# Performance work log

Hardware: AMD Instinct MI355X
Metric: run time of the kernel (lower is better)

## Reference

```python
import jax, jax.numpy as jnp
import numpy as np

EPS_CB = 1e-6   # ConvBlock BN eps (partial(nn.BatchNorm2d, eps=1e-6))
EPS_BN = 1e-5   # default nn.BatchNorm2d / BatchNorm1d eps


def conv2d(x, w, stride=1, pad=0):
    return jax.lax.conv_general_dilated(
        x, w, (stride, stride), [(pad, pad), (pad, pad)],
        dimension_numbers=('NCHW', 'OIHW', 'NCHW'))


def bn2d(x, g, b, m, v, eps):
    inv = (g / jnp.sqrt(v + eps)).reshape(1, -1, 1, 1)
    return (x - m.reshape(1, -1, 1, 1)) * inv + b.reshape(1, -1, 1, 1)


def setup_inputs() -> dict:
    key = jax.random.key(0)
    ks = iter(jax.random.split(key, 40))
    B, C, H, W = 16, 512, 64, 64
    K = 64                 # num_codes (hard-coded to 64 in __init__)
    c4 = C // 4            # bottleneck width in ConvBlock (expansion=4)

    def w_(shape, scale=0.05):
        return jax.random.normal(next(ks), shape, jnp.float32) * scale

    def bnp(n):
        return (jax.random.uniform(next(ks), (n,), jnp.float32, 0.5, 1.5),  # gamma
                w_((n,), 0.05),                                            # beta
                w_((n,), 0.05),                                            # running mean
                jax.random.uniform(next(ks), (n,), jnp.float32, 0.5, 1.5)) # running var

    g1, b1, m1, v1 = bnp(c4)
    g2, b2, m2, v2 = bnp(c4)
    g3, b3, m3, v3 = bnp(C)
    gr, br, mr, vr = bnp(C)
    gl, bl, ml, vl = bnp(C)
    ge, be, me, ve = bnp(K)

    std = 1.0 / np.sqrt(K * C)
    inp = {
        'x': jax.random.normal(next(ks), (B, C, H, W), jnp.float32),
        # ConvBlock
        'w1': w_((c4, C, 1, 1)), 'g1': g1, 'b1': b1, 'm1': m1, 'v1': v1,
        'w2': w_((c4, c4, 3, 3)), 'g2': g2, 'b2': b2, 'm2': m2, 'v2': v2,
        'w3': w_((C, c4, 1, 1)), 'g3': g3, 'b3': b3, 'm3': m3, 'v3': v3,
        'wr': w_((C, C, 1, 1)), 'gr': gr, 'br': br, 'mr': mr, 'vr': vr,
        # LVC 1x1 conv + BN2d
        'wl': w_((C, C, 1, 1)), 'gl': gl, 'bl': bl, 'ml': ml, 'vl': vl,
        # Encoding
        'codewords': jax.random.uniform(next(ks), (K, C), jnp.float32, -std, std),
        'scale': jax.random.uniform(next(ks), (K,), jnp.float32, -1.0, 0.0),
        # BN1d over codes
        'ge': ge, 'be': be, 'me': me, 've': ve,
        # fc gate
        'wfc': w_((C, C)), 'bfc': w_((C,), 0.05),
    }
    return inp


def lvc_forward(x, w1, g1, b1, m1, v1, w2, g2, b2, m2, v2, w3, g3, b3, m3, v3,
                wr, gr, br, mr, vr, wl, gl, bl, ml, vl, codewords, scale,
                ge, be, me, ve, wfc, bfc):
    # ---- ConvBlock (bottleneck with 1x1 residual), eval-mode BN ----
    h = jax.nn.relu(bn2d(conv2d(x, w1), g1, b1, m1, v1, EPS_CB))
    h = jax.nn.relu(bn2d(conv2d(h, w2, pad=1), g2, b2, m2, v2, EPS_CB))
    h = jax.nn.relu(bn2d(conv2d(h, w3), g3, b3, m3, v3, EPS_CB))
    res = bn2d(conv2d(x, wr), gr, br, mr, vr, EPS_CB)
    x1 = h + res                                   # (B, C, H, W)

    # ---- LVC: 1x1 conv + BN + ReLU ----
    y = jax.nn.relu(bn2d(conv2d(x1, wl), gl, bl, ml, vl, EPS_BN))

    # ---- Encoding: scaled L2 -> softmax over codes -> aggregate ----
    B, C, H, W = y.shape
    xf = y.reshape(B, C, H * W).transpose(0, 2, 1)     # (B, N, C)
    x_sq = jnp.sum(xf * xf, axis=-1, keepdims=True)    # (B, N, 1)
    c_sq = jnp.sum(codewords * codewords, axis=-1)     # (K,)
    xc = jnp.einsum('bnc,kc->bnk', xf, codewords)      # (B, N, K)
    dist = scale * (x_sq - 2.0 * xc + c_sq)            # (B, N, K)
    A = jax.nn.softmax(dist, axis=2)                   # assignment weights
    # sum_n A[b,n,k] * (x[b,n,:] - codewords[k,:])  -> (B, K, C)
    enc = jnp.einsum('bnk,bnc->bkc', A, xf) - A.sum(axis=1)[..., None] * codewords

    # ---- BN1d over num_codes dim + ReLU + mean over codes ----
    inv = (ge / jnp.sqrt(ve + EPS_BN)).reshape(1, -1, 1)
    enc = (enc - me.reshape(1, -1, 1)) * inv + be.reshape(1, -1, 1)
    en = jax.nn.relu(enc).mean(axis=1)                 # (B, C)

    # ---- SE-style gate ----
    gam = jax.nn.sigmoid(en @ wfc.T + bfc)             # (B, C)
    gate = gam.reshape(B, C, 1, 1)
    return jax.nn.relu(x1 + x1 * gate)


def reference(x, w1, g1, b1, m1, v1, w2, g2, b2, m2, v2, w3, g3, b3, m3, v3,
              wr, gr, br, mr, vr, wl, gl, bl, ml, vl, codewords, scale,
              ge, be, me, ve, wfc, bfc):
    return lvc_forward(x, w1, g1, b1, m1, v1, w2, g2, b2, m2, v2,
                       w3, g3, b3, m3, v3, wr, gr, br, mr, vr,
                       wl, gl, bl, ml, vl, codewords, scale,
                       ge, be, me, ve, wfc, bfc)
```

## Files before the change

### kernel.cpp

```cpp
#include <hip/hip_runtime.h>
#include <math.h>

typedef float f32x4 __attribute__((ext_vector_type(4)));
typedef short s16x8 __attribute__((ext_vector_type(8)));
typedef unsigned short u16x4 __attribute__((ext_vector_type(4)));

#define HW 4096
#define CCH 512
#define NK 64
#define EPAD 136

#define C_XB   0ULL
#define C_H2   67108864ULL
#define C_H1P  83886080ULL
#define C_X1B  83886080ULL
#define C_YB   0ULL
#define C_AHI  67108864ULL
#define C_ALO  75497472ULL
#define C_ASUM 150994944ULL
#define C_GAM  150999040ULL
#define C_MISC 151031808ULL
#define C_W1F  151048192ULL
#define C_W2F  151179264ULL
#define C_W3B  151474176ULL
#define C_WRB  151605248ULL
#define C_WLB  152129536ULL
#define C_PE   152653824ULL

#define MS_S1 0
#define MS_T1 128
#define MS_S2 256
#define MS_T2 384
#define MS_S3 512
#define MS_T3 1024
#define MS_SR 1536
#define MS_TR 2048
#define MS_SL 2560
#define MS_TL 3072
#define MS_SE 3584
#define MS_TE 3648
#define MS_CSQ 3712

__device__ __forceinline__ float b2f(unsigned short u) {
  unsigned int x = ((unsigned int)u) << 16;
  return __builtin_bit_cast(float, x);
}
__device__ __forceinline__ unsigned short f2b(float f) {
  unsigned int i = __builtin_bit_cast(unsigned int, f);
  i += 0x7fffu + ((i >> 16) & 1u);
  return (unsigned short)(i >> 16);
}

__global__ void prep_kernel(
    const float* __restrict__ g1, const float* __restrict__ b1, const float* __restrict__ m1, const float* __restrict__ v1,
    const float* __restrict__ g2, const float* __restrict__ b2, const float* __restrict__ m2, const float* __restrict__ v2,
    const float* __restrict__ g3, const float* __restrict__ b3, const float* __restrict__ m3, const float* __restrict__ v3,
    const float* __restrict__ gr, const float* __restrict__ br, const float* __restrict__ mr, const float* __restrict__ vr,
    const float* __restrict__ gl, const float* __restrict__ bl, const float* __restrict__ ml, const float* __restrict__ vl,
    const float* __restrict__ ge, const float* __restrict__ be, const float* __restrict__ me, const float* __restrict__ ve,
    const float* __restrict__ cw, float* __restrict__ misc)
{
  const int t = threadIdx.x;
  if (t < 128) {
    float s = g1[t] * rsqrtf(v1[t] + 1e-6f);
    misc[MS_S1 + t] = s; misc[MS_T1 + t] = b1[t] - m1[t] * s;
    s = g2[t] * rsqrtf(v2[t] + 1e-6f);
    misc[MS_S2 + t] = s; misc[MS_T2 + t] = b2[t] - m2[t] * s;
  }
  for (int c = t; c < 512; c += 256) {
    float s = g3[c] * rsqrtf(v3[c] + 1e-6f);
    misc[MS_S3 + c] = s; misc[MS_T3 + c] = b3[c] - m3[c] * s;
    s = gr[c] * rsqrtf(vr[c] + 1e-6f);
    misc[MS_SR + c] = s; misc[MS_TR + c] = br[c] - mr[c] * s;
    s = gl[c] * rsqrtf(vl[c] + 1e-5f);
    misc[MS_SL + c] = s; misc[MS_TL + c] = bl[c] - ml[c] * s;
  }
  if (t < 64) {
    float s = ge[t] * rsqrtf(ve[t] + 1e-5f);
    misc[MS_SE + t] = s; misc[MS_TE + t] = be[t] - me[t] * s;
    float acc = 0.f;
    for (int c = 0; c < 512; ++c) { float v = cw[t * 512 + c]; acc += v * v; }
    misc[MS_CSQ + t] = acc;
  }
}

__global__ void fold_bf16_kernel(const float* __restrict__ w, const float* __restrict__ s,
                                 unsigned short* __restrict__ out, int total, int kper)
{
  int i = blockIdx.x * 256 + threadIdx.x;
  if (i < total) out[i] = f2b(w[i] * s[i / kper]);
}

__global__ void fold_w2_kernel(const float* __restrict__ w2, const float* __restrict__ s,
                               unsigned short* __restrict__ out)
{
  int j = blockIdx.x * 256 + threadIdx.x;
  if (j < 147456) {
    int m = j / 1152, r = j - m * 1152;
    int tp = r >> 7, ci = r & 127;
    out[j] = f2b(w2[m * 1152 + ci * 9 + tp] * s[m]);
  }
}

__global__ __launch_bounds__(256) void tr_kernel(const float* __restrict__ x,
                                                 unsigned short* __restrict__ xb)
{
  __shared__ float T[64][65];
  const int b = blockIdx.z, c0 = blockIdx.y * 64, n0 = blockIdx.x * 64;
  const int t = threadIdx.x;
  const int rr = t >> 4, cc = (t & 15) * 4;
#pragma unroll
  for (int rep = 0; rep < 4; ++rep) {
    const int cr = rep * 16 + rr;
    const float4 v = *(const float4*)(x + ((size_t)(b * 512 + c0 + cr)) * 4096 + n0 + cc);
    T[cr][cc + 0] = v.x; T[cr][cc + 1] = v.y; T[cr][cc + 2] = v.z; T[cr][cc + 3] = v.w;
  }
  __syncthreads();
#pragma unroll
  for (int rep = 0; rep < 4; ++rep) {
    const int nr = rep * 16 + rr;
    u16x4 o;
    o[0] = f2b(T[cc + 0][nr]); o[1] = f2b(T[cc + 1][nr]);
    o[2] = f2b(T[cc + 2][nr]); o[3] = f2b(T[cc + 3][nr]);
    *(u16x4*)(xb + ((size_t)(b * 4096 + n0 + nr)) * 512 + c0 + cc) = o;
  }
}


template<int BMODE>
__device__ __forceinline__ void run_phase(
    const unsigned short* __restrict__ Wp,
    const unsigned short* __restrict__ Xb,
    const int K, const int tid, const int n0,
    unsigned short* __restrict__ As, unsigned short* __restrict__ Bs,
    f32x4 acc[4][4])
{
  const int lane = tid & 63;
  const int wv = tid >> 6, wm = wv >> 1, wn = wv & 1;

  const int ko = tid & 3;
  const int r0 = tid >> 2;
  const int r1 = 64 + r0;

  const unsigned short* aS0 = Wp + (size_t)r0 * K + ko * 8;
  const unsigned short* aS1 = Wp + (size_t)r1 * K + ko * 8;
  const int slot0 = (((r0 >> 4) * 64) + ko * 16 + (r0 & 15)) * 8;
  const int slot1 = (((r1 >> 4) * 64) + ko * 16 + (r1 & 15)) * 8;

  const unsigned short* bS0 = nullptr;
  const unsigned short* bS1 = nullptr;
  size_t bBase0 = 0, bBase1 = 0;
  if constexpr (BMODE == 0) {
    bS0 = Xb + (size_t)(n0 + r0) * K + ko * 8;
    bS1 = Xb + (size_t)(n0 + r1) * K + ko * 8;
  } else {
    const int pg0 = n0 + r0, pg1 = n0 + r1;
    bBase0 = (size_t)((pg0 >> 6) * 66 + (pg0 & 63)) * 128 + ko * 8;
    bBase1 = (size_t)((pg1 >> 6) * 66 + (pg1 & 63)) * 128 + ko * 8;
  }

  s16x8 a0, a1, b0, b1;
  auto LOADC = [&](int kt) {
    __builtin_memcpy(&a0, aS0 + kt, 16);
    __builtin_memcpy(&a1, aS1 + kt, 16);
    if constexpr (BMODE == 0) {
      __builtin_memcpy(&b0, bS0 + kt, 16);
      __builtin_memcpy(&b1, bS1 + kt, 16);
    } else {
      const int tap = kt >> 7;
      const int ky = tap / 3, kx = tap - ky * 3;
      const int off = (ky * 66 + kx) * 128 + (kt & 127);
      __builtin_memcpy(&b0, Xb + bBase0 + off, 16);
      __builtin_memcpy(&b1, Xb + bBase1 + off, 16);
    }
  };

  LOADC(0);
  *(s16x8*)(As + slot0) = a0; *(s16x8*)(As + slot1) = a1;
  *(s16x8*)(Bs + slot0) = b0; *(s16x8*)(Bs + slot1) = b1;
  __syncthreads();

  int cur = 0;
  for (int kt = 0; kt < K; kt += 32) {
    const bool more = (kt + 32) < K;
    if (more) LOADC(kt + 32);

    const unsigned short* Ac = As + cur * 4096;
    const unsigned short* Bc = Bs + cur * 4096;
    s16x8 afr[4], bfr[4];
#pragma unroll
    for (int i = 0; i < 4; ++i)
      afr[i] = *(const s16x8*)(Ac + (size_t)((wm * 4 + i) * 64 + lane) * 8);
#pragma unroll
    for (int j = 0; j < 4; ++j)
      bfr[j] = *(const s16x8*)(Bc + (size_t)((wn * 4 + j) * 64 + lane) * 8);
#pragma unroll
    for (int i = 0; i < 4; ++i)
#pragma unroll
      for (int j = 0; j < 4; ++j)
        acc[i][j] = __builtin_amdgcn_mfma_f32_16x16x32_bf16(afr[i], bfr[j], acc[i][j], 0, 0, 0);

    if (more) {
      const int nx = (cur ^ 1) * 4096;
      *(s16x8*)(As + nx + slot0) = a0; *(s16x8*)(As + nx + slot1) = a1;
      *(s16x8*)(Bs + nx + slot0) = b0; *(s16x8*)(Bs + nx + slot1) = b1;
    }
    __syncthreads();
    cur ^= 1;
  }
}

template<int BMODE, bool DUAL>
__global__ __launch_bounds__(256) void mgemm_kernel(
    const unsigned short* __restrict__ W0, const unsigned short* __restrict__ X0,
    const int K0, const long long xbs0,
    const unsigned short* __restrict__ W1, const unsigned short* __restrict__ X1,
    const int Kp1, const long long xbs1,
    const float* __restrict__ biasMid, const float* __restrict__ biasOut,
    const int omode, const int reluF, const int ldm,
    unsigned short* __restrict__ outB, const long long obsB)
{
  __shared__ __align__(16) unsigned short smem[128 * EPAD];
  unsigned short* As = smem;
  unsigned short* Bs = smem + 8192;

  const int tid = threadIdx.x;
  const int b = blockIdx.z;
  const int n0 = blockIdx.x * 128;
  const int m0 = blockIdx.y * 128;
  const int lane = tid & 63, wv = tid >> 6, wm = wv >> 1, wn = wv & 1;
  const int q = lane >> 4, mm = lane & 15;

  f32x4 acc[4][4];
#pragma unroll
  for (int i = 0; i < 4; ++i)
#pragma unroll
    for (int j = 0; j < 4; ++j) acc[i][j] = (f32x4){0.f, 0.f, 0.f, 0.f};

  run_phase<BMODE>(W0 + (size_t)m0 * K0, X0 + (size_t)b * xbs0, K0, tid, n0, As, Bs, acc);

  if constexpr (DUAL) {
#pragma unroll
    for (int i = 0; i < 4; ++i) {
      const int mb = m0 + wm * 64 + i * 16 + q * 4;
#pragma unroll
      for (int r = 0; r < 4; ++r) {
        const float bm = biasMid[mb + r];
#pragma unroll
        for (int j = 0; j < 4; ++j) acc[i][j][r] = fmaxf(acc[i][j][r] + bm, 0.f);
      }
    }
    run_phase<0>(W1 + (size_t)m0 * Kp1, X1 + (size_t)b * xbs1, Kp1, tid, n0, As, Bs, acc);
  }

  __syncthreads();
  if (omode == 3) {
#pragma unroll
    for (int i = 0; i < 4; ++i) {
      const int chb = wm * 64 + i * 16 + q * 4;
#pragma unroll
      for (int r = 0; r < 4; ++r) {
        const float bo = biasOut[m0 + chb + r];
#pragma unroll
        for (int j = 0; j < 4; ++j) {
          const int px = wn * 64 + j * 16 + mm;
          float v = acc[i][j][r] + bo;
          if (reluF) v = fmaxf(v, 0.f);
          smem[(size_t)(chb + r) * EPAD + px] = f2b(v);
        }
      }
    }
    __syncthreads();
    const int ch = tid >> 1, half = tid & 1;
    const unsigned short* src = smem + (size_t)ch * EPAD + half * 64;
    unsigned short* dst = outB + (size_t)b * obsB + (size_t)(m0 + ch) * HW + n0 + half * 64;
#pragma unroll
    for (int r = 0; r < 8; ++r) {
      s16x8 v;
      __builtin_memcpy(&v, src + r * 8, 16);
      *(s16x8*)(dst + r * 8) = v;
    }
  } else {
#pragma unroll
    for (int i = 0; i < 4; ++i) {
      const int chb = wm * 64 + i * 16 + q * 4;
      float bo[4];
#pragma unroll
      for (int r = 0; r < 4; ++r) bo[r] = biasOut[m0 + chb + r];
#pragma unroll
      for (int j = 0; j < 4; ++j) {
        const int px = wn * 64 + j * 16 + mm;
        u16x4 o;
#pragma unroll
        for (int r = 0; r < 4; ++r) {
          float v = acc[i][j][r] + bo[r];
          if (reluF) v = fmaxf(v, 0.f);
          o[r] = f2b(v);
        }
        *(u16x4*)(smem + (size_t)px * EPAD + chb) = o;
      }
    }
    __syncthreads();
    const int px = tid >> 1, half = tid & 1;
    const unsigned short* src = smem + (size_t)px * EPAD + half * 64;
    size_t dstoff;
    if (omode == 1) {
      dstoff = (size_t)b * obsB + (size_t)(n0 + px) * ldm + m0 + half * 64;
    } else {
      const int hp = ((n0 + px) >> 6) + 1, wp = ((n0 + px) & 63) + 1;
      dstoff = (size_t)b * obsB + ((size_t)hp * 66 + wp) * 128 + m0 + half * 64;
    }
    unsigned short* dst = outB + dstoff;
#pragma unroll
    for (int r = 0; r < 8; ++r) {
      s16x8 v;
      __builtin_memcpy(&v, src + r * 8, 16);
      *(s16x8*)(dst + r * 8) = v;
    }
  }
}

__global__ __launch_bounds__(256) void assign_kernel(
    const unsigned short* __restrict__ Yv, const float* __restrict__ cw, const float* __restrict__ scale,
    const float* __restrict__ misc, unsigned short* __restrict__ Ahi, unsigned short* __restrict__ Alo)
{
  __shared__ float Cs[16][64];
  __shared__ float Ys[16][64];
  __shared__ float dist[64][65];
  __shared__ float red[4][64];
  __shared__ float xsq[64];
  __shared__ float scl[64];
  __shared__ float csq[64];
  const int tid = threadIdx.x;
  const int b  = blockIdx.y;
  const int n0 = blockIdx.x * 64;
  if (tid < 64) { scl[tid] = scale[tid]; csq[tid] = misc[MS_CSQ + tid]; }
  const unsigned short* __restrict__ Yb = Yv + (size_t)b * CCH * HW;
  const int tr = tid >> 4, tc = tid & 15;
  const int lc_k = tid >> 2, lc_c = (tid & 3) * 4;
  const int ly_c0 = tid >> 6, ly_n = tid & 63;

  float acc[4][4];
#pragma unroll
  for (int i = 0; i < 4; ++i)
#pragma unroll
    for (int j = 0; j < 4; ++j) acc[i][j] = 0.f;
  float sq = 0.f;

  for (int c0 = 0; c0 < 512; c0 += 16) {
    const float4 cv = *(const float4*)(cw + (size_t)lc_k * 512 + c0 + lc_c);
    float yv[4];
#pragma unroll
    for (int rr = 0; rr < 4; ++rr)
      yv[rr] = b2f(Yb[(size_t)(c0 + ly_c0 + rr * 4) * HW + n0 + ly_n]);
    __syncthreads();
    Cs[lc_c + 0][lc_k] = cv.x;
    Cs[lc_c + 1][lc_k] = cv.y;
    Cs[lc_c + 2][lc_k] = cv.z;
    Cs[lc_c + 3][lc_k] = cv.w;
#pragma unroll
    for (int rr = 0; rr < 4; ++rr) {
      Ys[ly_c0 + rr * 4][ly_n] = yv[rr];
      sq += yv[rr] * yv[rr];
    }
    __syncthreads();
#pragma unroll
    for (int ct = 0; ct < 16; ++ct) {
      float rk[4], rn[4];
#pragma unroll
      for (int i = 0; i < 4; ++i) rk[i] = Cs[ct][tr * 4 + i];
#pragma unroll
      for (int j = 0; j < 4; ++j) rn[j] = Ys[ct][tc * 4 + j];
#pragma unroll
      for (int i = 0; i < 4; ++i)
#pragma unroll
        for (int j = 0; j < 4; ++j) acc[i][j] += rk[i] * rn[j];
    }
  }
  __syncthreads();
  red[ly_c0][ly_n] = sq;
  __syncthreads();
  if (tid < 64) xsq[tid] = red[0][tid] + red[1][tid] + red[2][tid] + red[3][tid];
  __syncthreads();
#pragma unroll
  for (int i = 0; i < 4; ++i)
#pragma unroll
    for (int j = 0; j < 4; ++j) {
      const int k = tr * 4 + i, n = tc * 4 + j;
      dist[k][n] = scl[k] * (xsq[n] - 2.f * acc[i][j] + csq[k]);
    }
  __syncthreads();
  const int qq = tid >> 6, n = tid & 63;
  float mx = -3.0e38f;
#pragma unroll
  for (int kk = 0; kk < 16; ++kk) mx = fmaxf(mx, dist[qq * 16 + kk][n]);
  red[qq][n] = mx;
  __syncthreads();
  mx = fmaxf(fmaxf(red[0][n], red[1][n]), fmaxf(red[2][n], red[3][n]));
  __syncthreads();
  float sum = 0.f;
#pragma unroll
  for (int kk = 0; kk < 16; ++kk) {
    const float e = __expf(dist[qq * 16 + kk][n] - mx);
    dist[qq * 16 + kk][n] = e;
    sum += e;
  }
  red[qq][n] = sum;
  __syncthreads();
  sum = red[0][n] + red[1][n] + red[2][n] + red[3][n];
  const float inv = 1.f / sum;
  const size_t base = (size_t)b * NK * HW + n0 + n;
#pragma unroll
  for (int kk = 0; kk < 16; ++kk) {
    const float a = dist[qq * 16 + kk][n] * inv;
    const unsigned short hi = f2b(a);
    const float rem = a - b2f(hi);
    Ahi[base + (size_t)(qq * 16 + kk) * HW] = hi;
    Alo[base + (size_t)(qq * 16 + kk) * HW] = f2b(rem);
  }
}

__global__ void asum_kernel(const unsigned short* __restrict__ Ahi,
                            const unsigned short* __restrict__ Alo, float* __restrict__ asum)
{
  const int bk = blockIdx.x;
  const unsigned short* __restrict__ rh = Ahi + (size_t)bk * HW;
  const unsigned short* __restrict__ rl = Alo + (size_t)bk * HW;
  const int t = threadIdx.x;
  float p = 0.f;
  for (int i = t * 8; i < HW; i += 2048) {
    s16x8 h, l;
    __builtin_memcpy(&h, rh + i, 16);
    __builtin_memcpy(&l, rl + i, 16);
#pragma unroll
    for (int e = 0; e < 8; ++e)
      p += b2f((unsigned short)h[e]) + b2f((unsigned short)l[e]);
  }
  __shared__ float sm[256];
  sm[t] = p;
  __syncthreads();
  for (int s = 128; s > 0; s >>= 1) {
    if (t < s) sm[t] += sm[t + s];
    __syncthreads();
  }
  if (t == 0) asum[bk] = sm[0];
}

__global__ __launch_bounds__(256) void enc_mfma_kernel(
    const unsigned short* __restrict__ Ahi, const unsigned short* __restrict__ Alo,
    const unsigned short* __restrict__ Yv, float* __restrict__ pe)
{
  __shared__ __align__(16) unsigned short AHs[2048];
  __shared__ __align__(16) unsigned short ALs[2048];
  __shared__ __align__(16) unsigned short Bs[4096];
  const int tid = threadIdx.x;
  const int ncol = blockIdx.x, nc = blockIdx.y, b = blockIdx.z;
  const int lane = tid & 63, wv = tid >> 6;
  const int q = lane >> 4, mm = lane & 15;

  const int ko = tid & 3;
  const int r  = tid >> 2;
  const size_t aoff = ((size_t)b * NK + r) * HW + nc * 1024 + ko * 8;
  const unsigned short* ahS = Ahi + aoff;
  const unsigned short* alS = Alo + aoff;
  const int slotA = (((r >> 4) * 64) + ko * 16 + (r & 15)) * 8;
  const unsigned short* b0S = Yv + ((size_t)b * CCH + ncol * 128 + r) * HW + nc * 1024 + ko * 8;
  const unsigned short* b1S = b0S + (size_t)64 * HW;
  const int slotB0 = (((r >> 4) * 64) + ko * 16 + (r & 15)) * 8;
  const int slotB1 = ((((r + 64) >> 4) * 64) + ko * 16 + (r & 15)) * 8;

  f32x4 acc[4][2];
#pragma unroll
  for (int i = 0; i < 4; ++i)
#pragma unroll
    for (int j = 0; j < 2; ++j) acc[i][j] = (f32x4){0.f, 0.f, 0.f, 0.f};

  for (int kt = 0; kt < 1024; kt += 32) {
    s16x8 ah, al, y0, y1;
    __builtin_memcpy(&ah, ahS + kt, 16);
    __builtin_memcpy(&al, alS + kt, 16);
    __builtin_memcpy(&y0, b0S + kt, 16);
    __builtin_memcpy(&y1, b1S + kt, 16);
    __syncthreads();
    *(s16x8*)(AHs + slotA) = ah;
    *(s16x8*)(ALs + slotA) = al;
    *(s16x8*)(Bs + slotB0) = y0;
    *(s16x8*)(Bs + slotB1) = y1;
    __syncthreads();

    s16x8 afh[4], afl[4], bfr[2];
#pragma unroll
    for (int i = 0; i < 4; ++i) {
      afh[i] = *(const s16x8*)(AHs + (size_t)(i * 64 + lane) * 8);
      afl[i] = *(const s16x8*)(ALs + (size_t)(i * 64 + lane) * 8);
    }
#pragma unroll
    for (int j = 0; j < 2; ++j)
      bfr[j] = *(const s16x8*)(Bs + (size_t)((wv * 2 + j) * 64 + lane) * 8);
#pragma unroll
    for (int i = 0; i < 4; ++i)
#pragma unroll
      for (int j = 0; j < 2; ++j) {
        acc[i][j] = __builtin_amdgcn_mfma_f32_16x16x32_bf16(afh[i], bfr[j], acc[i][j], 0, 0, 0);
        acc[i][j] = __builtin_amdgcn_mfma_f32_16x16x32_bf16(afl[i], bfr[j], acc[i][j], 0, 0, 0);
      }
  }

  float* __restrict__ peb = pe + ((size_t)(b * 4 + nc) * NK) * CCH;
#pragma unroll
  for (int i = 0; i < 4; ++i)
#pragma unroll
    for (int j = 0; j < 2; ++j) {
      const int c = ncol * 128 + (wv * 2 + j) * 16 + mm;
#pragma unroll
      for (int rr = 0; rr < 4; ++rr) {
        const int k = i * 16 + q * 4 + rr;
        peb[(size_t)k * CCH + c] = acc[i][j][rr];
      }
    }
}

__global__ __launch_bounds__(256) void engate_kernel(
    const float* __restrict__ pe, const float* __restrict__ asum, const float* __restrict__ cw,
    const float* __restrict__ misc, const float* __restrict__ wfc, const float* __restrict__ bfc,
    float* __restrict__ gam)
{
  const int b = blockIdx.x;
  const int t = threadIdx.x;
  __shared__ float asum_s[64], se_s[64], te_s[64];
  __shared__ __align__(16) float en_s[512];
  if (t < 64) {
    asum_s[t] = asum[b * 64 + t];
    se_s[t]   = misc[MS_SE + t];
    te_s[t]   = misc[MS_TE + t];
  }
  __syncthreads();
  for (int rep = 0; rep < 2; ++rep) {
    const int c = t + rep * 256;
    float en = 0.f;
    const float* __restrict__ peb = pe + (size_t)b * 4 * NK * CCH + c;
    for (int k = 0; k < 64; ++k) {
      const float ps = peb[(size_t)k * CCH] + peb[(size_t)(64 + k) * CCH] +
                       peb[(size_t)(128 + k) * CCH] + peb[(size_t)(192 + k) * CCH];
      float v = ps - asum_s[k] * cw[k * 512 + c];
      v = v * se_s[k] + te_s[k];
      en += fmaxf(v, 0.f);
    }
    en_s[c] = en * (1.f / 64.f);
  }
  __syncthreads();
  for (int rep = 0; rep < 2; ++rep) {
    const int i = t + rep * 256;
    float a = bfc[i];
    const float4* __restrict__ wrow = (const float4*)(wfc + (size_t)i * 512);
    const float4* __restrict__ ev = (const float4*)en_s;
    for (int j = 0; j < 128; ++j) {
      const float4 w4 = wrow[j];
      const float4 e4 = ev[j];
      a += w4.x * e4.x + w4.y * e4.y + w4.z * e4.z + w4.w * e4.w;
    }
    gam[b * 512 + i] = 1.f / (1.f + __expf(-a));
  }
}

__global__ __launch_bounds__(256) void fingate_kernel(
    const unsigned short* __restrict__ x1b, const float* __restrict__ gam,
    float* __restrict__ out)
{
  __shared__ float T[64][65];
  const int b = blockIdx.z, c0 = blockIdx.y * 64, n0 = blockIdx.x * 64;
  const int t = threadIdx.x;
  const int rr = t >> 4, cc = (t & 15) * 4;
#pragma unroll
  for (int rep = 0; rep < 4; ++rep) {
    const int pr = rep * 16 + rr;
    u16x4 v = *(const u16x4*)(x1b + ((size_t)(b * 4096 + n0 + pr)) * 512 + c0 + cc);
    T[cc + 0][pr] = b2f(v[0]);
    T[cc + 1][pr] = b2f(v[1]);
    T[cc + 2][pr] = b2f(v[2]);
    T[cc + 3][pr] = b2f(v[3]);
  }
  __syncthreads();
#pragma unroll
  for (int rep = 0; rep < 4; ++rep) {
    const int cr = rep * 16 + rr;
    const float g = 1.f + gam[b * 512 + c0 + cr];
    float4 o;
    o.x = fmaxf(T[cr][cc + 0] * g, 0.f);
    o.y = fmaxf(T[cr][cc + 1] * g, 0.f);
    o.z = fmaxf(T[cr][cc + 2] * g, 0.f);
    o.w = fmaxf(T[cr][cc + 3] * g, 0.f);
    *(float4*)(out + ((size_t)(b * 512 + c0 + cr)) * 4096 + n0 + cc) = o;
  }
}

extern "C" void kernel_launch(void* const* d_in, const int* in_sizes, int n_in,
                              void* d_out, int out_size, void* d_ws, size_t ws_size,
                              hipStream_t stream)
{
  const float* x  = (const float*)d_in[0];
  const float* w1 = (const float*)d_in[1];
  const float* g1 = (const float*)d_in[2];
  const float* b1 = (const float*)d_in[3];
  const float* m1 = (const float*)d_in[4];
  const float* v1 = (const float*)d_in[5];
  const float* w2 = (const float*)d_in[6];
  const float* g2 = (const float*)d_in[7];
  const float* b2 = (const float*)d_in[8];
  const float* m2 = (const float*)d_in[9];
  const float* v2 = (const float*)d_in[10];
  const float* w3 = (const float*)d_in[11];
  const float* g3 = (const float*)d_in[12];
  const float* b3 = (const float*)d_in[13];
  const float* m3 = (const float*)d_in[14];
  const float* v3 = (const float*)d_in[15];
  const float* wr = (const float*)d_in[16];
  const float* gr = (const float*)d_in[17];
  const float* br = (const float*)d_in[18];
  const float* mr = (const float*)d_in[19];
  const float* vr = (const float*)d_in[20];
  const float* wl = (const float*)d_in[21];
  const float* gl = (const float*)d_in[22];
  const float* bl = (const float*)d_in[23];
  const float* ml = (const float*)d_in[24];
  const float* vl = (const float*)d_in[25];
  const float* cw = (const float*)d_in[26];
  const float* scale = (const float*)d_in[27];
  const float* ge = (const float*)d_in[28];
  const float* be = (const float*)d_in[29];
  const float* me = (const float*)d_in[30];
  const float* ve = (const float*)d_in[31];
  const float* wfc = (const float*)d_in[32];
  const float* bfc = (const float*)d_in[33];

  char* wsb = (char*)d_ws;
  unsigned short* xb  = (unsigned short*)(wsb + C_XB);
  unsigned short* h2  = (unsigned short*)(wsb + C_H2);
  unsigned short* h1p = (unsigned short*)(wsb + C_H1P);
  unsigned short* x1b = (unsigned short*)(wsb + C_X1B);
  unsigned short* yb  = (unsigned short*)(wsb + C_YB);
  unsigned short* Ahi = (unsigned short*)(wsb + C_AHI);
  unsigned short* Alo = (unsigned short*)(wsb + C_ALO);
  float* pe   = (float*)(wsb + C_PE);
  float* asum = (float*)(wsb + C_ASUM);
  float* gam  = (float*)(wsb + C_GAM);
  float* misc = (float*)(wsb + C_MISC);
  unsigned short* w1f = (unsigned short*)(wsb + C_W1F);
  unsigned short* w2f = (unsigned short*)(wsb + C_W2F);
  unsigned short* w3b = (unsigned short*)(wsb + C_W3B);
  unsigned short* wrb = (unsigned short*)(wsb + C_WRB);
  unsigned short* wlb = (unsigned short*)(wsb + C_WLB);

  prep_kernel<<<1, 256, 0, stream>>>(g1, b1, m1, v1, g2, b2, m2, v2, g3, b3, m3, v3,
                                     gr, br, mr, vr, gl, bl, ml, vl, ge, be, me, ve,
                                     cw, misc);
  fold_bf16_kernel<<<256, 256, 0, stream>>>(w1, misc + MS_S1, w1f, 65536, 512);
  fold_w2_kernel<<<576, 256, 0, stream>>>(w2, misc + MS_S2, w2f);
  fold_bf16_kernel<<<256, 256, 0, stream>>>(w3, misc + MS_S3, w3b, 65536, 128);
  fold_bf16_kernel<<<1024, 256, 0, stream>>>(wr, misc + MS_SR, wrb, 262144, 512);
  fold_bf16_kernel<<<1024, 256, 0, stream>>>(wl, misc + MS_SL, wlb, 262144, 512);

  tr_kernel<<<dim3(64, 8, 16), 256, 0, stream>>>(x, xb);
  hipMemsetAsync(h1p, 0, 17842176, stream);

  mgemm_kernel<0, false><<<dim3(32, 1, 16), 256, 0, stream>>>(
      w1f, xb, 512, 4096LL * 512, nullptr, nullptr, 0, 0,
      nullptr, misc + MS_T1, 0, 1, 128, h1p, 4356LL * 128);
  mgemm_kernel<1, false><<<dim3(32, 1, 16), 256, 0, stream>>>(
      w2f, h1p, 1152, 4356LL * 128, nullptr, nullptr, 0, 0,
      nullptr, misc + MS_T2, 1, 1, 128, h2, 4096LL * 128);
  mgemm_kernel<0, true><<<dim3(32, 4, 16), 256, 0, stream>>>(
      w3b, h2, 128, 4096LL * 128, wrb, xb, 512, 4096LL * 512,
      misc + MS_T3, misc + MS_TR, 1, 0, 512, x1b, 4096LL * 512);
  mgemm_kernel<0, false><<<dim3(32, 4, 16), 256, 0, stream>>>(
      wlb, x1b, 512, 4096LL * 512, nullptr, nullptr, 0, 0,
      nullptr, misc + MS_TL, 3, 1, 0, yb, 512LL * 4096);

  assign_kernel<<<dim3(64, 16), 256, 0, stream>>>(yb, cw, scale, misc, Ahi, Alo);
  asum_kernel<<<1024, 256, 0, stream>>>(Ahi, Alo, asum);
  enc_mfma_kernel<<<dim3(4, 4, 16), 256, 0, stream>>>(Ahi, Alo, yb, pe);
  engate_kernel<<<16, 256, 0, stream>>>(pe, asum, cw, misc, wfc, bfc, gam);
  fingate_kernel<<<dim3(64, 8, 16), 256, 0, stream>>>(x1b, gam, (float*)d_out);
}
```

Baseline: 461.2 us.

## Widen GEMM block tile to 128x256 pixels with two-phase epilogue

Each GEMM block now covers 256 pixels instead of 128, so every warp accumulates a 4x8 grid of MFMA tiles and each A fragment is reused across twice as many B fragments. The B tile staging buffers grow to match, and the epilogue is split into two 128-pixel phases that reuse the existing shared-memory staging area. The goal is fewer global and LDS loads per MFMA. In exchange the accumulator footprint doubles, which raises register pressure and can lower occupancy, and the small M=128 GEMMs now launch only 256 blocks, which may underfill the GPU.

```diff
diff --git a/kernel.cpp b/kernel.cpp
--- a/kernel.cpp
+++ b/kernel.cpp
@@ -127,87 +127,104 @@
 }
 
 
+__device__ __forceinline__ void mfma_step(const unsigned short* __restrict__ Ac,
+                                          const unsigned short* __restrict__ Bc,
+                                          int lane, int wm, int wn, f32x4 acc[4][8])
+{
+  s16x8 afr[4], bfr[8];
+#pragma unroll
+  for (int i = 0; i < 4; ++i)
+    afr[i] = *(const s16x8*)(Ac + (size_t)((wm * 4 + i) * 64 + lane) * 8);
+#pragma unroll
+  for (int j = 0; j < 8; ++j)
+    bfr[j] = *(const s16x8*)(Bc + (size_t)((wn * 8 + j) * 64 + lane) * 8);
+#pragma unroll
+  for (int i = 0; i < 4; ++i)
+#pragma unroll
+    for (int j = 0; j < 8; ++j)
+      acc[i][j] = __builtin_amdgcn_mfma_f32_16x16x32_bf16(afr[i], bfr[j], acc[i][j], 0, 0, 0);
+}
+
 template<int BMODE>
 __device__ __forceinline__ void run_phase(
     const unsigned short* __restrict__ Wp,
     const unsigned short* __restrict__ Xb,
     const int K, const int tid, const int n0,
     unsigned short* __restrict__ As, unsigned short* __restrict__ Bs,
-    f32x4 acc[4][4])
+    f32x4 acc[4][8])
 {
   const int lane = tid & 63;
   const int wv = tid >> 6, wm = wv >> 1, wn = wv & 1;
 
   const int ko = tid & 3;
-  const int r0 = tid >> 2;
-  const int r1 = 64 + r0;
-
-  const unsigned short* aS0 = Wp + (size_t)r0 * K + ko * 8;
-  const unsigned short* aS1 = Wp + (size_t)r1 * K + ko * 8;
-  const int slot0 = (((r0 >> 4) * 64) + ko * 16 + (r0 & 15)) * 8;
-  const int slot1 = (((r1 >> 4) * 64) + ko * 16 + (r1 & 15)) * 8;
-
-  const unsigned short* bS0 = nullptr;
-  const unsigned short* bS1 = nullptr;
-  size_t bBase0 = 0, bBase1 = 0;
-  if constexpr (BMODE == 0) {
-    bS0 = Xb + (size_t)(n0 + r0) * K + ko * 8;
-    bS1 = Xb + (size_t)(n0 + r1) * K + ko * 8;
-  } else {
-    const int pg0 = n0 + r0, pg1 = n0 + r1;
-    bBase0 = (size_t)((pg0 >> 6) * 66 + (pg0 & 63)) * 128 + ko * 8;
-    bBase1 = (size_t)((pg1 >> 6) * 66 + (pg1 & 63)) * 128 + ko * 8;
-  }
-
-  s16x8 a0, a1, b0, b1;
-  auto LOADC = [&](int kt) {
-    __builtin_memcpy(&a0, aS0 + kt, 16);
-    __builtin_memcpy(&a1, aS1 + kt, 16);
+  const int rt = tid >> 2;
+  const unsigned short* aS0 = Wp + (size_t)rt * K + ko * 8;
+  const unsigned short* aS1 = Wp + (size_t)(64 + rt) * K + ko * 8;
+  const int slA0 = (((rt >> 4) * 64) + ko * 16 + (rt & 15)) * 8;
+  const int slA1 = ((((64 + rt) >> 4) * 64) + ko * 16 + (rt & 15)) * 8;
+
+  const unsigned short* bS[4];
+  size_t bBase[4];
+  int slB[4];
+#pragma unroll
+  for (int u = 0; u < 4; ++u) {
+    const int r = rt + u * 64;
+    slB[u] = (((r >> 4) * 64) + ko * 16 + (r & 15)) * 8;
     if constexpr (BMODE == 0) {
-      __builtin_memcpy(&b0, bS0 + kt, 16);
-      __builtin_memcpy(&b1, bS1 + kt, 16);
+      bS[u] = Xb + (size_t)(n0 + r) * K + ko * 8;
+      bBase[u] = 0;
     } else {
-      const int tap = kt >> 7;
-      const int ky = tap / 3, kx = tap - ky * 3;
-      const int off = (ky * 66 + kx) * 128 + (kt & 127);
-      __builtin_memcpy(&b0, Xb + bBase0 + off, 16);
-      __builtin_memcpy(&b1, Xb + bBase1 + off, 16);
-    }
-  };
+      const int pg = n0 + r;
+      bS[u] = nullptr;
+      bBase[u] = (size_t)((pg >> 6) * 66 + (pg & 63)) * 128 + ko * 8;
+    }
+  }
+
+  s16x8 a0, a1, bb0, bb1, bb2, bb3;
+#define LOADC(kt)                                                 \
+  {                                                               \
+    __builtin_memcpy(&a0, aS0 + (kt), 16);                        \
+    __builtin_memcpy(&a1, aS1 + (kt), 16);                        \
+    if constexpr (BMODE == 0) {                                   \
+      __builtin_memcpy(&bb0, bS[0] + (kt), 16);                   \
+      __builtin_memcpy(&bb1, bS[1] + (kt), 16);                   \
+      __builtin_memcpy(&bb2, bS[2] + (kt), 16);                   \
+      __builtin_memcpy(&bb3, bS[3] + (kt), 16);                   \
+    } else {                                                      \
+      const int tap_ = (kt) >> 7;                                 \
+      const int ky_ = tap_ / 3, kx_ = tap_ - ky_ * 3;             \
+      const int off_ = (ky_ * 66 + kx_) * 128 + ((kt) & 127);     \
+      __builtin_memcpy(&bb0, Xb + bBase[0] + off_, 16);           \
+      __builtin_memcpy(&bb1, Xb + bBase[1] + off_, 16);           \
+      __builtin_memcpy(&bb2, Xb + bBase[2] + off_, 16);           \
+      __builtin_memcpy(&bb3, Xb + bBase[3] + off_, 16);           \
+    }                                                             \
+  }
+#define WRITEC(Abuf, Bbuf)                                        \
+  {                                                               \
+    *(s16x8*)((Abuf) + slA0) = a0;                                \
+    *(s16x8*)((Abuf) + slA1) = a1;                                \
+    *(s16x8*)((Bbuf) + slB[0]) = bb0;                             \
+    *(s16x8*)((Bbuf) + slB[1]) = bb1;                             \
+    *(s16x8*)((Bbuf) + slB[2]) = bb2;                             \
+    *(s16x8*)((Bbuf) + slB[3]) = bb3;                             \
+  }
 
   LOADC(0);
-  *(s16x8*)(As + slot0) = a0; *(s16x8*)(As + slot1) = a1;
-  *(s16x8*)(Bs + slot0) = b0; *(s16x8*)(Bs + slot1) = b1;
+  WRITEC(As, Bs);
   __syncthreads();
 
   int cur = 0;
   for (int kt = 0; kt < K; kt += 32) {
     const bool more = (kt + 32) < K;
     if (more) LOADC(kt + 32);
-
-    const unsigned short* Ac = As + cur * 4096;
-    const unsigned short* Bc = Bs + cur * 4096;
-    s16x8 afr[4], bfr[4];
-#pragma unroll
-    for (int i = 0; i < 4; ++i)
-      afr[i] = *(const s16x8*)(Ac + (size_t)((wm * 4 + i) * 64 + lane) * 8);
-#pragma unroll
-    for (int j = 0; j < 4; ++j)
-      bfr[j] = *(const s16x8*)(Bc + (size_t)((wn * 4 + j) * 64 + lane) * 8);
-#pragma unroll
-    for (int i = 0; i < 4; ++i)
-#pragma unroll
-      for (int j = 0; j < 4; ++j)
-        acc[i][j] = __builtin_amdgcn_mfma_f32_16x16x32_bf16(afr[i], bfr[j], acc[i][j], 0, 0, 0);
-
-    if (more) {
-      const int nx = (cur ^ 1) * 4096;
-      *(s16x8*)(As + nx + slot0) = a0; *(s16x8*)(As + nx + slot1) = a1;
-      *(s16x8*)(Bs + nx + slot0) = b0; *(s16x8*)(Bs + nx + slot1) = b1;
-    }
+    mfma_step(As + cur * 4096, Bs + cur * 8192, lane, wm, wn, acc);
+    if (more) WRITEC(As + (cur ^ 1) * 4096, Bs + (cur ^ 1) * 8192);
     __syncthreads();
     cur ^= 1;
   }
+#undef LOADC
+#undef WRITEC
 }
 
 template<int BMODE, bool DUAL>
@@ -220,22 +237,22 @@
     const int omode, const int reluF, const int ldm,
     unsigned short* __restrict__ outB, const long long obsB)
 {
-  __shared__ __align__(16) unsigned short smem[128 * EPAD];
+  __shared__ __align__(16) unsigned short smem[24576];
   unsigned short* As = smem;
   unsigned short* Bs = smem + 8192;
 
   const int tid = threadIdx.x;
   const int b = blockIdx.z;
-  const int n0 = blockIdx.x * 128;
+  const int n0 = blockIdx.x * 256;
   const int m0 = blockIdx.y * 128;
   const int lane = tid & 63, wv = tid >> 6, wm = wv >> 1, wn = wv & 1;
   const int q = lane >> 4, mm = lane & 15;
 
-  f32x4 acc[4][4];
+  f32x4 acc[4][8];
 #pragma unroll
   for (int i = 0; i < 4; ++i)
 #pragma unroll
-    for (int j = 0; j < 4; ++j) acc[i][j] = (f32x4){0.f, 0.f, 0.f, 0.f};
+    for (int j = 0; j < 8; ++j) acc[i][j] = (f32x4){0.f, 0.f, 0.f, 0.f};
 
   run_phase<BMODE>(W0 + (size_t)m0 * K0, X0 + (size_t)b * xbs0, K0, tid, n0, As, Bs, acc);
 
@@ -247,75 +264,84 @@
       for (int r = 0; r < 4; ++r) {
         const float bm = biasMid[mb + r];
 #pragma unroll
-        for (int j = 0; j < 4; ++j) acc[i][j][r] = fmaxf(acc[i][j][r] + bm, 0.f);
+        for (int j = 0; j < 8; ++j) acc[i][j][r] = fmaxf(acc[i][j][r] + bm, 0.f);
       }
     }
     run_phase<0>(W1 + (size_t)m0 * Kp1, X1 + (size_t)b * xbs1, Kp1, tid, n0, As, Bs, acc);
   }
 
   __syncthreads();
-  if (omode == 3) {
-#pragma unroll
-    for (int i = 0; i < 4; ++i) {
-      const int chb = wm * 64 + i * 16 + q * 4;
-#pragma unroll
-      for (int r = 0; r < 4; ++r) {
-        const float bo = biasOut[m0 + chb + r];
-#pragma unroll
-        for (int j = 0; j < 4; ++j) {
-          const int px = wn * 64 + j * 16 + mm;
-          float v = acc[i][j][r] + bo;
-          if (reluF) v = fmaxf(v, 0.f);
-          smem[(size_t)(chb + r) * EPAD + px] = f2b(v);
+  for (int ph = 0; ph < 2; ++ph) {
+    if (omode == 3) {
+      if (wn == ph) {
+#pragma unroll
+        for (int i = 0; i < 4; ++i) {
+          const int chb = wm * 64 + i * 16 + q * 4;
+#pragma unroll
+          for (int r = 0; r < 4; ++r) {
+            const float bo = biasOut[m0 + chb + r];
+#pragma unroll
+            for (int j = 0; j < 8; ++j) {
+              const int px = j * 16 + mm;
+              float v = acc[i][j][r] + bo;
+              if (reluF) v = fmaxf(v, 0.f);
+              smem[(size_t)(chb + r) * EPAD + px] = f2b(v);
+            }
+          }
         }
       }
-    }
-    __syncthreads();
-    const int ch = tid >> 1, half = tid & 1;
-    const unsigned short* src = smem + (size_t)ch * EPAD + half * 64;
-    unsigned short* dst = outB + (size_t)b * obsB + (size_t)(m0 + ch) * HW + n0 + half * 64;
-#pragma unroll
-    for (int r = 0; r < 8; ++r) {
-      s16x8 v;
-      __builtin_memcpy(&v, src + r * 8, 16);
-      *(s16x8*)(dst + r * 8) = v;
-    }
-  } else {
-#pragma unroll
-    for (int i = 0; i < 4; ++i) {
-      const int chb = wm * 64 + i * 16 + q * 4;
-      float bo[4];
-#pragma unroll
-      for (int r = 0; r < 4; ++r) bo[r] = biasOut[m0 + chb + r];
-#pragma unroll
-      for (int j = 0; j < 4; ++j) {
-        const int px = wn * 64 + j * 16 + mm;
-        u16x4 o;
-#pragma unroll
-        for (int r = 0; r < 4; ++r) {
-          float v = acc[i][j][r] + bo[r];
-          if (reluF) v = fmaxf(v, 0.f);
-          o[r] = f2b(v);
+      __syncthreads();
+      const int ch = tid >> 1, half = tid & 1;
+      const unsigned short* src = smem + (size_t)ch * EPAD + half * 64;
+      unsigned short* dst = outB + (size_t)b * obsB + (size_t)(m0 + ch) * HW + n0 + ph * 128 + half * 64;
+#pragma unroll
+      for (int r = 0; r < 8; ++r) {
+        s16x8 v;
+        __builtin_memcpy(&v, src + r * 8, 16);
+        *(s16x8*)(dst + r * 8) = v;
+      }
+      __syncthreads();
+    } else {
+      if (wn == ph) {
+#pragma unroll
+        for (int i = 0; i < 4; ++i) {
+          const int chb = wm * 64 + i * 16 + q * 4;
+          float bo[4];
+#pragma unroll
+          for (int r = 0; r < 4; ++r) bo[r] = biasOut[m0 + chb + r];
+#pragma unroll
+          for (int j = 0; j < 8; ++j) {
+            const int px = j * 16 + mm;
+            u16x4 o;
+#pragma unroll
+            for (int r = 0; r < 4; ++r) {
+              float v = acc[i][j][r] + bo[r];
+              if (reluF) v = fmaxf(v, 0.f);
+              o[r] = f2b(v);
+            }
+            *(u16x4*)(smem + (size_t)px * EPAD + chb) = o;
+          }
         }
-        *(u16x4*)(smem + (size_t)px * EPAD + chb) = o;
       }
-    }
-    __syncthreads();
-    const int px = tid >> 1, half = tid & 1;
-    const unsigned short* src = smem + (size_t)px * EPAD + half * 64;
-    size_t dstoff;
-    if (omode == 1) {
-      dstoff = (size_t)b * obsB + (size_t)(n0 + px) * ldm + m0 + half * 64;
-    } else {
-      const int hp = ((n0 + px) >> 6) + 1, wp = ((n0 + px) & 63) + 1;
-      dstoff = (size_t)b * obsB + ((size_t)hp * 66 + wp) * 128 + m0 + half * 64;
-    }
-    unsigned short* dst = outB + dstoff;
-#pragma unroll
-    for (int r = 0; r < 8; ++r) {
-      s16x8 v;
-      __builtin_memcpy(&v, src + r * 8, 16);
-      *(s16x8*)(dst + r * 8) = v;
+      __syncthreads();
+      const int px = tid >> 1, half = tid & 1;
+      const int gpx = n0 + ph * 128 + px;
+      const unsigned short* src = smem + (size_t)px * EPAD + half * 64;
+      size_t dstoff;
+      if (omode == 1) {
+        dstoff = (size_t)b * obsB + (size_t)gpx * ldm + m0 + half * 64;
+      } else {
+        const int hp = (gpx >> 6) + 1, wp = (gpx & 63) + 1;
+        dstoff = (size_t)b * obsB + ((size_t)hp * 66 + wp) * 128 + m0 + half * 64;
+      }
+      unsigned short* dst = outB + dstoff;
+#pragma unroll
+      for (int r = 0; r < 8; ++r) {
+        s16x8 v;
+        __builtin_memcpy(&v, src + r * 8, 16);
+        *(s16x8*)(dst + r * 8) = v;
+      }
+      __syncthreads();
     }
   }
 }
@@ -663,16 +689,16 @@
   tr_kernel<<<dim3(64, 8, 16), 256, 0, stream>>>(x, xb);
   hipMemsetAsync(h1p, 0, 17842176, stream);
 
-  mgemm_kernel<0, false><<<dim3(32, 1, 16), 256, 0, stream>>>(
+  mgemm_kernel<0, false><<<dim3(16, 1, 16), 256, 0, stream>>>(
       w1f, xb, 512, 4096LL * 512, nullptr, nullptr, 0, 0,
       nullptr, misc + MS_T1, 0, 1, 128, h1p, 4356LL * 128);
-  mgemm_kernel<1, false><<<dim3(32, 1, 16), 256, 0, stream>>>(
+  mgemm_kernel<1, false><<<dim3(16, 1, 16), 256, 0, stream>>>(
       w2f, h1p, 1152, 4356LL * 128, nullptr, nullptr, 0, 0,
       nullptr, misc + MS_T2, 1, 1, 128, h2, 4096LL * 128);
-  mgemm_kernel<0, true><<<dim3(32, 4, 16), 256, 0, stream>>>(
+  mgemm_kernel<0, true><<<dim3(16, 4, 16), 256, 0, stream>>>(
       w3b, h2, 128, 4096LL * 128, wrb, xb, 512, 4096LL * 512,
       misc + MS_T3, misc + MS_TR, 1, 0, 512, x1b, 4096LL * 512);
-  mgemm_kernel<0, false><<<dim3(32, 4, 16), 256, 0, stream>>>(
+  mgemm_kernel<0, false><<<dim3(16, 4, 16), 256, 0, stream>>>(
       wlb, x1b, 512, 4096LL * 512, nullptr, nullptr, 0, 0,
       nullptr, misc + MS_TL, 3, 1, 0, yb, 512LL * 4096);
 
```

Measured after the change: 514.4 us. 11.5% more time.

## Compute code-assignment distances with bf16 MFMA using hi/lo split codewords

Applied to the files above, without the earlier changes.

Replaces the scalar FP32 x·codeword dot product in the assignment kernel with MFMA 16x16x32 bf16 instructions. Codewords are split into bf16 high and low parts by a new fold kernel, so accuracy on the codeword side is kept close to the FP32 path, while Y is already bf16. The squared norm of each pixel is accumulated during the load loop. This removes most of the FMA work in assignment at the cost of an extra tiny kernel and a new LDS transpose layout.

```diff
diff --git a/kernel.cpp b/kernel.cpp
--- a/kernel.cpp
+++ b/kernel.cpp
@@ -26,6 +26,8 @@
 #define C_WRB  151605248ULL
 #define C_WLB  152129536ULL
 #define C_PE   152653824ULL
+#define C_CWH  161042432ULL
+#define C_CWL  161107968ULL
 
 #define MS_S1 0
 #define MS_T1 128
@@ -102,6 +104,18 @@
   }
 }
 
+__global__ void fold_cw_kernel(const float* __restrict__ cw,
+                               unsigned short* __restrict__ ch, unsigned short* __restrict__ cl)
+{
+  int i = blockIdx.x * 256 + threadIdx.x;
+  if (i < 32768) {
+    const float v = cw[i];
+    const unsigned short hi = f2b(v);
+    ch[i] = hi;
+    cl[i] = f2b(v - b2f(hi));
+  }
+}
+
 __global__ __launch_bounds__(256) void tr_kernel(const float* __restrict__ x,
                                                  unsigned short* __restrict__ xb)
 {
@@ -125,7 +139,6 @@
     *(u16x4*)(xb + ((size_t)(b * 4096 + n0 + nr)) * 512 + c0 + cc) = o;
   }
 }
-
 
 template<int BMODE>
 __device__ __forceinline__ void run_phase(
@@ -320,76 +333,85 @@
   }
 }
 
-__global__ __launch_bounds__(256) void assign_kernel(
-    const unsigned short* __restrict__ Yv, const float* __restrict__ cw, const float* __restrict__ scale,
-    const float* __restrict__ misc, unsigned short* __restrict__ Ahi, unsigned short* __restrict__ Alo)
-{
-  __shared__ float Cs[16][64];
-  __shared__ float Ys[16][64];
+__global__ __launch_bounds__(256) void assign_mfma_kernel(
+    const unsigned short* __restrict__ Yv,
+    const unsigned short* __restrict__ cwh, const unsigned short* __restrict__ cwl,
+    const float* __restrict__ scale, const float* __restrict__ misc,
+    unsigned short* __restrict__ Ahi, unsigned short* __restrict__ Alo)
+{
+  __shared__ __align__(16) unsigned short Bt[64][36];
+  __shared__ float xpart[64][33];
   __shared__ float dist[64][65];
   __shared__ float red[4][64];
   __shared__ float xsq[64];
   __shared__ float scl[64];
   __shared__ float csq[64];
   const int tid = threadIdx.x;
-  const int b  = blockIdx.y;
+  const int b = blockIdx.y;
   const int n0 = blockIdx.x * 64;
+  const int lane = tid & 63, wv = tid >> 6;
+  const int q = lane >> 4, mm = lane & 15;
   if (tid < 64) { scl[tid] = scale[tid]; csq[tid] = misc[MS_CSQ + tid]; }
-  const unsigned short* __restrict__ Yb = Yv + (size_t)b * CCH * HW;
-  const int tr = tid >> 4, tc = tid & 15;
-  const int lc_k = tid >> 2, lc_c = (tid & 3) * 4;
-  const int ly_c0 = tid >> 6, ly_n = tid & 63;
-
-  float acc[4][4];
-#pragma unroll
-  for (int i = 0; i < 4; ++i)
-#pragma unroll
-    for (int j = 0; j < 4; ++j) acc[i][j] = 0.f;
-  float sq = 0.f;
-
-  for (int c0 = 0; c0 < 512; c0 += 16) {
-    const float4 cv = *(const float4*)(cw + (size_t)lc_k * 512 + c0 + lc_c);
-    float yv[4];
-#pragma unroll
-    for (int rr = 0; rr < 4; ++rr)
-      yv[rr] = b2f(Yb[(size_t)(c0 + ly_c0 + rr * 4) * HW + n0 + ly_n]);
+
+  const int g = tid >> 5, ci = tid & 31;
+  const unsigned short* ySrc = Yv + (size_t)b * CCH * HW + (size_t)ci * HW + n0 + g * 8;
+  const unsigned short* ahP = cwh + (size_t)(wv * 16 + mm) * 512 + q * 8;
+  const unsigned short* alP = cwl + (size_t)(wv * 16 + mm) * 512 + q * 8;
+
+  f32x4 acc[4];
+#pragma unroll
+  for (int j = 0; j < 4; ++j) acc[j] = (f32x4){0.f, 0.f, 0.f, 0.f};
+  float xp[8] = {0.f, 0.f, 0.f, 0.f, 0.f, 0.f, 0.f, 0.f};
+
+  for (int kc = 0; kc < 16; ++kc) {
+    s16x8 v8;
+    __builtin_memcpy(&v8, ySrc + (size_t)(kc * 32) * HW, 16);
+    s16x8 ah, al;
+    __builtin_memcpy(&ah, ahP + kc * 32, 16);
+    __builtin_memcpy(&al, alP + kc * 32, 16);
     __syncthreads();
-    Cs[lc_c + 0][lc_k] = cv.x;
-    Cs[lc_c + 1][lc_k] = cv.y;
-    Cs[lc_c + 2][lc_k] = cv.z;
-    Cs[lc_c + 3][lc_k] = cv.w;
-#pragma unroll
-    for (int rr = 0; rr < 4; ++rr) {
-      Ys[ly_c0 + rr * 4][ly_n] = yv[rr];
-      sq += yv[rr] * yv[rr];
+#pragma unroll
+    for (int e = 0; e < 8; ++e) {
+      Bt[g * 8 + e][ci] = (unsigned short)v8[e];
+      const float f = b2f((unsigned short)v8[e]);
+      xp[e] += f * f;
     }
     __syncthreads();
 #pragma unroll
-    for (int ct = 0; ct < 16; ++ct) {
-      float rk[4], rn[4];
-#pragma unroll
-      for (int i = 0; i < 4; ++i) rk[i] = Cs[ct][tr * 4 + i];
-#pragma unroll
-      for (int j = 0; j < 4; ++j) rn[j] = Ys[ct][tc * 4 + j];
-#pragma unroll
-      for (int i = 0; i < 4; ++i)
-#pragma unroll
-        for (int j = 0; j < 4; ++j) acc[i][j] += rk[i] * rn[j];
-    }
-  }
-  __syncthreads();
-  red[ly_c0][ly_n] = sq;
+    for (int j = 0; j < 4; ++j) {
+      s16x8 bf;
+      __builtin_memcpy(&bf, &Bt[j * 16 + mm][q * 8], 16);
+      acc[j] = __builtin_amdgcn_mfma_f32_16x16x32_bf16(ah, bf, acc[j], 0, 0, 0);
+      acc[j] = __builtin_amdgcn_mfma_f32_16x16x32_bf16(al, bf, acc[j], 0, 0, 0);
+    }
+  }
+
+  __syncthreads();
+#pragma unroll
+  for (int e = 0; e < 8; ++e) xpart[g * 8 + e][ci] = xp[e];
+  __syncthreads();
+  {
+    const int px = tid >> 2, part = tid & 3;
+    float s = 0.f;
+#pragma unroll
+    for (int u = 0; u < 8; ++u) s += xpart[px][part * 8 + u];
+    red[part][px] = s;
+  }
   __syncthreads();
   if (tid < 64) xsq[tid] = red[0][tid] + red[1][tid] + red[2][tid] + red[3][tid];
   __syncthreads();
-#pragma unroll
-  for (int i = 0; i < 4; ++i)
-#pragma unroll
-    for (int j = 0; j < 4; ++j) {
-      const int k = tr * 4 + i, n = tc * 4 + j;
-      dist[k][n] = scl[k] * (xsq[n] - 2.f * acc[i][j] + csq[k]);
-    }
-  __syncthreads();
+
+#pragma unroll
+  for (int j = 0; j < 4; ++j) {
+    const int n = j * 16 + mm;
+#pragma unroll
+    for (int r = 0; r < 4; ++r) {
+      const int k = wv * 16 + q * 4 + r;
+      dist[k][n] = scl[k] * (xsq[n] - 2.f * acc[j][r] + csq[k]);
+    }
+  }
+  __syncthreads();
+
   const int qq = tid >> 6, n = tid & 63;
   float mx = -3.0e38f;
 #pragma unroll
@@ -650,6 +672,8 @@
   unsigned short* w3b = (unsigned short*)(wsb + C_W3B);
   unsigned short* wrb = (unsigned short*)(wsb + C_WRB);
   unsigned short* wlb = (unsigned short*)(wsb + C_WLB);
+  unsigned short* cwh = (unsigned short*)(wsb + C_CWH);
+  unsigned short* cwl = (unsigned short*)(wsb + C_CWL);
 
   prep_kernel<<<1, 256, 0, stream>>>(g1, b1, m1, v1, g2, b2, m2, v2, g3, b3, m3, v3,
                                      gr, br, mr, vr, gl, bl, ml, vl, ge, be, me, ve,
@@ -659,6 +683,7 @@
   fold_bf16_kernel<<<256, 256, 0, stream>>>(w3, misc + MS_S3, w3b, 65536, 128);
   fold_bf16_kernel<<<1024, 256, 0, stream>>>(wr, misc + MS_SR, wrb, 262144, 512);
   fold_bf16_kernel<<<1024, 256, 0, stream>>>(wl, misc + MS_SL, wlb, 262144, 512);
+  fold_cw_kernel<<<128, 256, 0, stream>>>(cw, cwh, cwl);
 
   tr_kernel<<<dim3(64, 8, 16), 256, 0, stream>>>(x, xb);
   hipMemsetAsync(h1p, 0, 17842176, stream);
@@ -676,7 +701,7 @@
       wlb, x1b, 512, 4096LL * 512, nullptr, nullptr, 0, 0,
       nullptr, misc + MS_TL, 3, 1, 0, yb, 512LL * 4096);
 
-  assign_kernel<<<dim3(64, 16), 256, 0, stream>>>(yb, cw, scale, misc, Ahi, Alo);
+  assign_mfma_kernel<<<dim3(64, 16), 256, 0, stream>>>(yb, cwh, cwl, scale, misc, Ahi, Alo);
   asum_kernel<<<1024, 256, 0, stream>>>(Ahi, Alo, asum);
   enc_mfma_kernel<<<dim3(4, 4, 16), 256, 0, stream>>>(Ahi, Alo, yb, pe);
   engate_kernel<<<16, 256, 0, stream>>>(pe, asum, cw, misc, wfc, bfc, gam);
```

After: 428.3 us. -7.1%, faster.
